# Kernel optimization log

Measured on AMD Instinct MI355X. Metric: run time of the kernel, lower is better.

## Reference

```python
import jax, jax.numpy as jnp
import numpy as np

N_EMBD = 1024
N_HEAD = 16
HEAD_DIM = N_EMBD // N_HEAD


def setup_inputs() -> dict:
    key = jax.random.key(0)
    ks = jax.random.split(key, 5)
    B, S = 2, 2048
    scale = 0.02
    return {
        "hidden_states": jax.random.normal(ks[0], (B, S, N_EMBD), dtype=jnp.float32),
        "w_attn": jax.random.normal(ks[1], (N_EMBD, 3 * N_EMBD), dtype=jnp.float32) * scale,
        "b_attn": jnp.zeros((3 * N_EMBD,), dtype=jnp.float32),
        "w_proj": jax.random.normal(ks[2], (N_EMBD, N_EMBD), dtype=jnp.float32) * scale,
        "b_proj": jnp.zeros((N_EMBD,), dtype=jnp.float32),
    }


def reference(hidden_states, w_attn, b_attn, w_proj, b_proj):
    B, S, _ = hidden_states.shape
    qkv = hidden_states @ w_attn + b_attn                     # [B,S,3E]
    q, k, v = jnp.split(qkv, 3, axis=-1)                      # each [B,S,E]

    def split_heads(t):  # [B,S,E] -> [B,H,S,D]
        return t.reshape(B, S, N_HEAD, HEAD_DIM).transpose(0, 2, 1, 3)

    q, k, v = split_heads(q), split_heads(k), split_heads(v)

    scores = jnp.einsum("bhqd,bhkd->bhqk", q, k) / np.sqrt(HEAD_DIM).astype(np.float32)
    causal = jnp.tril(jnp.ones((S, S), dtype=bool))
    scores = jnp.where(causal[None, None], scores, jnp.float32(-jnp.inf))
    attn = jax.nn.softmax(scores, axis=-1)                    # [B,H,S,S]
    out = jnp.einsum("bhqk,bhkd->bhqd", attn, v)              # [B,H,S,D]
    out = out.transpose(0, 2, 1, 3).reshape(B, S, N_EMBD)     # merge heads
    out = out @ w_proj + b_proj
    return out
```

## Files before the change

### kernel.cpp

```cpp
#include <hip/hip_runtime.h>
#include <hip/hip_bf16.h>


typedef __attribute__((ext_vector_type(4))) float  float4v;
typedef __attribute__((ext_vector_type(8))) short  short8v;
typedef __attribute__((ext_vector_type(4))) short  short4v;

#define ATT_SCALE 0.18033688011112042f

__device__ __forceinline__ short f2bf(float f) {
  union { float f; unsigned u; } v; v.f = f;
  unsigned r = v.u + 0x7fffu + ((v.u >> 16) & 1u);
  return (short)(r >> 16);
}
__device__ __forceinline__ float bf2f(short s) {
  union { unsigned u; float f; } v; v.u = ((unsigned)(unsigned short)s) << 16;
  return v.f;
}

__device__ __forceinline__ short4v pack_bf16x4(float a, float b, float c, float d) {
  unsigned x0 = __builtin_bit_cast(unsigned, a) + 0x8000u;
  unsigned x1 = __builtin_bit_cast(unsigned, b) + 0x8000u;
  unsigned x2 = __builtin_bit_cast(unsigned, c) + 0x8000u;
  unsigned x3 = __builtin_bit_cast(unsigned, d) + 0x8000u;
  union { unsigned u[2]; short4v s; } r;
  r.u[0] = __builtin_amdgcn_perm(x1, x0, 0x07060302);
  r.u[1] = __builtin_amdgcn_perm(x3, x2, 0x07060302);
  return r.s;
}

__device__ __forceinline__ short4v cvt_pk_bf16x4(float a, float b, float c, float d) {
  union { unsigned u[2]; short4v s; } r;
  asm("v_cvt_pk_bf16_f32 %0, %1, %2" : "=v"(r.u[0]) : "v"(a), "v"(b));
  asm("v_cvt_pk_bf16_f32 %0, %1, %2" : "=v"(r.u[1]) : "v"(c), "v"(d));
  return r.s;
}

__device__ __forceinline__ void gl_lds16(const void* g, void* l) {
  __builtin_amdgcn_global_load_lds(
      (const __attribute__((address_space(1))) unsigned*)g,
      (__attribute__((address_space(3))) unsigned*)l, 16, 0, 0);
}

__global__ __launch_bounds__(256) void prep_kernel(
    const float* __restrict__ hidden, const float* __restrict__ w_attn,
    const float* __restrict__ w_proj, short* __restrict__ hA,
    short* __restrict__ wqkvT, short* __restrict__ wprojT) {
  __shared__ float tile[32][33];
  const int bx = blockIdx.x, t = threadIdx.x;
  if (bx < 4096) {
    const size_t i = ((size_t)bx * 256 + t) * 4;
    float4v v = *(const float4v*)(hidden + i);
    short4v o;
    #pragma unroll
    for (int k = 0; k < 4; k++) o[k] = f2bf(v[k]);
    *(short4v*)(hA + i) = o;
    return;
  }
  const float* in; short* out; int R, C, cx, cy;
  if (bx < 4096 + 3072) {
    in = w_attn; out = wqkvT; R = 1024; C = 3072;
    cx = (bx - 4096) % 96; cy = (bx - 4096) / 96;
  } else {
    in = w_proj; out = wprojT; R = 1024; C = 1024;
    cx = (bx - 7168) % 32; cy = (bx - 7168) / 32;
  }
  const int tx = t & 31, ty = t >> 5;
  const int c0 = cx * 32, r0 = cy * 32;
  #pragma unroll
  for (int i = 0; i < 4; i++)
    tile[ty + i * 8][tx] = in[(size_t)(r0 + ty + i * 8) * C + c0 + tx];
  __syncthreads();
  #pragma unroll
  for (int i = 0; i < 4; i++) {
    const int cc = ty + i * 8;
    out[(size_t)(c0 + cc) * R + r0 + tx] = f2bf(tile[tx][cc]);
  }
}

__global__ __launch_bounds__(512, 2) void gemm_qkv256(
    const short* __restrict__ A, const short* __restrict__ Bt,
    const float* __restrict__ bias, short* __restrict__ qkv,
    short* __restrict__ vA)
{
  __shared__ short As[2][256][64];
  __shared__ short Bs[2][256][64];
  const int K = 1024;
  const int t = threadIdx.x;
  const int lane = t & 63, w = t >> 6;
  const int wm2 = w >> 2, wn4 = w & 3;
  const int l16 = lane & 15, quad = lane >> 4;
  const int e7 = l16 & 7;
  const int row0 = blockIdx.y * 256;
  const int col0 = blockIdx.x * 256;

  float4v acc[8][4] = {};

  const int srow = w * 8 + (lane >> 3);
  const int slog = (lane & 7) ^ (lane >> 3);
  const short* gA = A + (size_t)(row0 + srow) * K + slog * 8;
  const short* gB = Bt + (size_t)(col0 + srow) * K + slog * 8;
  const int sdst = (lane & 7) * 8;

  auto stageA = [&](int b, int qd, int kt) {
    gl_lds16(gA + (size_t)qd * 64 * K + kt * 64,
             &As[b][qd * 64 + w * 8 + (lane >> 3)][sdst]);
  };
  auto stageB = [&](int b, int qd, int kt) {
    gl_lds16(gB + (size_t)qd * 64 * K + kt * 64,
             &Bs[b][qd * 64 + w * 8 + (lane >> 3)][sdst]);
  };

  short8v af[4], bf0[4], bf1[4];
  auto ldA = [&](int b, int mh, int ks) {
    #pragma unroll
    for (int m = 0; m < 4; m++) {
      const int row = wm2 * 128 + mh * 64 + m * 16 + l16;
      af[m] = *(const short8v*)&As[b][row][((ks * 4 + quad) ^ e7) * 8];
    }
  };
  auto ldB = [&](short8v* bf, int b, int ks) {
    #pragma unroll
    for (int n = 0; n < 4; n++) {
      const int row = wn4 * 64 + n * 16 + l16;
      bf[n] = *(const short8v*)&Bs[b][row][((ks * 4 + quad) ^ e7) * 8];
    }
  };
  auto mm = [&](int mb, short8v* bf) {
    __builtin_amdgcn_s_setprio(1);
    #pragma unroll
    for (int m = 0; m < 4; m++)
      #pragma unroll
      for (int n = 0; n < 4; n++)
        acc[mb + m][n] =
            __builtin_amdgcn_mfma_f32_16x16x32_bf16(af[m], bf[n], acc[mb + m][n], 0, 0, 0);
    __builtin_amdgcn_s_setprio(0);
  };
  auto sync_mfma = [&]() {
    __builtin_amdgcn_sched_barrier(0);
    __builtin_amdgcn_s_barrier();
    asm volatile("s_waitcnt lgkmcnt(0)" ::: "memory");
    __builtin_amdgcn_sched_barrier(0);
  };
  auto endp = [&]() {
    __builtin_amdgcn_sched_barrier(0);
    __builtin_amdgcn_s_barrier();
    __builtin_amdgcn_sched_barrier(0);
  };

  #pragma unroll
  for (int qd = 0; qd < 4; qd++) stageA(0, qd, 0);
  #pragma unroll
  for (int qd = 0; qd < 4; qd++) stageB(0, qd, 0);
  #pragma unroll
  for (int qd = 0; qd < 4; qd++) stageB(1, qd, 1);
  asm volatile("s_waitcnt vmcnt(4)" ::: "memory");
  __builtin_amdgcn_s_barrier();
  __builtin_amdgcn_sched_barrier(0);

  const int NIT = K / 128;
  #pragma unroll 1
  for (int it = 0; it < NIT; it++) {
    const bool st = (it < NIT - 1);
    const int t1 = 2 * it + 1, t2 = 2 * it + 2, t3 = 2 * it + 3;

    ldA(0, 0, 0); ldB(bf0, 0, 0);
    stageA(1, 0, t1); stageA(1, 1, t1);
    sync_mfma(); mm(0, bf0); endp();
    ldA(0, 0, 1); ldB(bf1, 0, 1);
    stageA(1, 2, t1); stageA(1, 3, t1);
    sync_mfma(); mm(0, bf1); endp();
    ldA(0, 1, 0);
    if (st) { stageB(0, 0, t2); stageB(0, 1, t2); }
    sync_mfma(); mm(4, bf0); endp();
    ldA(0, 1, 1);
    if (st) { stageB(0, 2, t2); stageB(0, 3, t2); }
    if (st) asm volatile("s_waitcnt vmcnt(4)" ::: "memory");
    else    asm volatile("s_waitcnt vmcnt(0)" ::: "memory");
    sync_mfma(); mm(4, bf1); endp();

    ldA(1, 0, 0); ldB(bf0, 1, 0);
    if (st) { stageA(0, 0, t2); stageA(0, 1, t2); }
    sync_mfma(); mm(0, bf0); endp();
    ldA(1, 0, 1); ldB(bf1, 1, 1);
    if (st) { stageA(0, 2, t2); stageA(0, 3, t2); }
    sync_mfma(); mm(0, bf1); endp();
    ldA(1, 1, 0);
    if (st) { stageB(1, 0, t3); stageB(1, 1, t3); }
    sync_mfma(); mm(4, bf0); endp();
    ldA(1, 1, 1);
    if (st) { stageB(1, 2, t3); stageB(1, 3, t3); }
    if (st) asm volatile("s_waitcnt vmcnt(4)" ::: "memory");
    sync_mfma(); mm(4, bf1); endp();
  }

  if (col0 >= 2048) {
    const int b  = row0 >> 11;
    const int hh = ((col0 - 2048) >> 6) + wn4;
    #pragma unroll
    for (int ktl = 0; ktl < 2; ktl++) {
      const int kt = ((row0 & 2047) >> 6) + wm2 * 2 + ktl;
      short* vbase = vA + ((size_t)((b * 16 + hh) * 32 + kt) * 8) * 512;
      #pragma unroll
      for (int j = 0; j < 4; j++) {
        const float bv = bias[col0 + wn4 * 64 + j * 16 + l16];
        #pragma unroll
        for (int kwp = 0; kwp < 2; kwp++) {
          short8v s8;
          #pragma unroll
          for (int kw = 0; kw < 2; kw++) {
            const int mi = ktl * 4 + kwp * 2 + kw;
            short4v q4 = pack_bf16x4(acc[mi][j][0] + bv, acc[mi][j][1] + bv,
                                     acc[mi][j][2] + bv, acc[mi][j][3] + bv);
            #pragma unroll
            for (int r = 0; r < 4; r++) s8[kw * 4 + r] = q4[r];
          }
          *(short8v*)(vbase + ((size_t)(kwp * 4 + j) * 64 + lane) * 8) = s8;
        }
      }
    }
    return;
  }
  #pragma unroll
  for (int j = 0; j < 4; j++) {
    const int col = col0 + wn4 * 64 + j * 16 + l16;
    const float sc = (col < 1024) ? ATT_SCALE : 1.0f;
    const float bv = bias[col];
    #pragma unroll
    for (int mi = 0; mi < 8; mi++) {
      #pragma unroll
      for (int r = 0; r < 4; r++) {
        const int row = row0 + wm2 * 128 + mi * 16 + quad * 4 + r;
        qkv[(size_t)row * 3072 + col] = f2bf((acc[mi][j][r] + bv) * sc);
      }
    }
  }
}

__global__ __launch_bounds__(256, 2) void gemm_proj128(
    const short* __restrict__ A, const short* __restrict__ Bt,
    const float* __restrict__ bias, float* __restrict__ Cout)
{
  __shared__ short As[2][128][64];
  __shared__ short Bs[2][128][64];
  const int K = 1024;
  const int t = threadIdx.x;
  const int lane = t & 63, w = t >> 6;
  const int wm2 = w >> 1, wn2 = w & 1;
  const int l16 = lane & 15, quad = lane >> 4;
  const int e7 = l16 & 7;
  const int row0 = blockIdx.y * 128;
  const int col0 = blockIdx.x * 128;

  float4v acc[4][4] = {};

  const int srow = w * 8 + (lane >> 3);
  const int slog = (lane & 7) ^ (lane >> 3);
  const short* gA = A + (size_t)(row0 + srow) * K + slog * 8;
  const short* gB = Bt + (size_t)(col0 + srow) * K + slog * 8;
  const int sdst = (lane & 7) * 8;

  auto stageA = [&](int b, int qd, int kt) {
    gl_lds16(gA + (size_t)qd * 32 * K + kt * 64,
             &As[b][qd * 32 + w * 8 + (lane >> 3)][sdst]);
  };
  auto stageB = [&](int b, int qd, int kt) {
    gl_lds16(gB + (size_t)qd * 32 * K + kt * 64,
             &Bs[b][qd * 32 + w * 8 + (lane >> 3)][sdst]);
  };

  short8v af[2], bf0[4], bf1[4];
  auto ldA = [&](int b, int mh, int ks) {
    #pragma unroll
    for (int m = 0; m < 2; m++) {
      const int row = wm2 * 64 + mh * 32 + m * 16 + l16;
      af[m] = *(const short8v*)&As[b][row][((ks * 4 + quad) ^ e7) * 8];
    }
  };
  auto ldB = [&](short8v* bf, int b, int ks) {
    #pragma unroll
    for (int n = 0; n < 4; n++) {
      const int row = wn2 * 64 + n * 16 + l16;
      bf[n] = *(const short8v*)&Bs[b][row][((ks * 4 + quad) ^ e7) * 8];
    }
  };
  auto mm = [&](int mb, short8v* bf) {
    __builtin_amdgcn_s_setprio(1);
    #pragma unroll
    for (int m = 0; m < 2; m++)
      #pragma unroll
      for (int n = 0; n < 4; n++)
        acc[mb + m][n] =
            __builtin_amdgcn_mfma_f32_16x16x32_bf16(af[m], bf[n], acc[mb + m][n], 0, 0, 0);
    __builtin_amdgcn_s_setprio(0);
  };
  auto sync_mfma = [&]() {
    __builtin_amdgcn_sched_barrier(0);
    __builtin_amdgcn_s_barrier();
    asm volatile("s_waitcnt lgkmcnt(0)" ::: "memory");
    __builtin_amdgcn_sched_barrier(0);
  };
  auto endp = [&]() {
    __builtin_amdgcn_sched_barrier(0);
    __builtin_amdgcn_s_barrier();
    __builtin_amdgcn_sched_barrier(0);
  };

  #pragma unroll
  for (int qd = 0; qd < 4; qd++) stageA(0, qd, 0);
  #pragma unroll
  for (int qd = 0; qd < 4; qd++) stageB(0, qd, 0);
  #pragma unroll
  for (int qd = 0; qd < 4; qd++) stageB(1, qd, 1);
  asm volatile("s_waitcnt vmcnt(4)" ::: "memory");
  __builtin_amdgcn_s_barrier();
  __builtin_amdgcn_sched_barrier(0);

  const int NIT = K / 128;
  #pragma unroll 1
  for (int it = 0; it < NIT; it++) {
    const bool st = (it < NIT - 1);
    const int t1 = 2 * it + 1, t2 = 2 * it + 2, t3 = 2 * it + 3;

    ldA(0, 0, 0); ldB(bf0, 0, 0);
    stageA(1, 0, t1); stageA(1, 1, t1);
    sync_mfma(); mm(0, bf0); endp();
    ldA(0, 0, 1); ldB(bf1, 0, 1);
    stageA(1, 2, t1); stageA(1, 3, t1);
    sync_mfma(); mm(0, bf1); endp();
    ldA(0, 1, 0);
    if (st) { stageB(0, 0, t2); stageB(0, 1, t2); }
    sync_mfma(); mm(2, bf0); endp();
    ldA(0, 1, 1);
    if (st) { stageB(0, 2, t2); stageB(0, 3, t2); }
    if (st) asm volatile("s_waitcnt vmcnt(4)" ::: "memory");
    else    asm volatile("s_waitcnt vmcnt(0)" ::: "memory");
    sync_mfma(); mm(2, bf1); endp();

    ldA(1, 0, 0); ldB(bf0, 1, 0);
    if (st) { stageA(0, 0, t2); stageA(0, 1, t2); }
    sync_mfma(); mm(0, bf0); endp();
    ldA(1, 0, 1); ldB(bf1, 1, 1);
    if (st) { stageA(0, 2, t2); stageA(0, 3, t2); }
    sync_mfma(); mm(0, bf1); endp();
    ldA(1, 1, 0);
    if (st) { stageB(1, 0, t3); stageB(1, 1, t3); }
    sync_mfma(); mm(2, bf0); endp();
    ldA(1, 1, 1);
    if (st) { stageB(1, 2, t3); stageB(1, 3, t3); }
    if (st) asm volatile("s_waitcnt vmcnt(4)" ::: "memory");
    sync_mfma(); mm(2, bf1); endp();
  }

  #pragma unroll
  for (int j = 0; j < 4; j++) {
    const int col = col0 + wn2 * 64 + j * 16 + l16;
    const float bv = bias[col];
    #pragma unroll
    for (int mi = 0; mi < 4; mi++) {
      #pragma unroll
      for (int r = 0; r < 4; r++) {
        const int row = row0 + wm2 * 64 + mi * 16 + quad * 4 + r;
        Cout[(size_t)row * 1024 + col] = acc[mi][j][r] + bv;
      }
    }
  }
}

__global__ __launch_bounds__(64, 2) void attn_mfma(
    const short* __restrict__ qkv, const short* __restrict__ vA,
    short* __restrict__ P0, short* __restrict__ P1, float* __restrict__ lp)
{
  const int bh = blockIdx.x;
  const int b = bh >> 4, h = bh & 15;
  const int s = 79 - blockIdx.y;
  int qt = 0, sbase = 0;
  for (;;) { const int nc = (qt >> 3) + 1; if (s < sbase + nc) break; sbase += nc; qt++; }
  const int c = s - sbase;
  const int kt0  = c * 8;
  const int kend = min(qt + 1, kt0 + 8);

  const int lane = threadIdx.x & 63;
  const int l16 = lane & 15, quad = lane >> 4;

  const size_t base = (size_t)b * 2048 * 3072;
  const int qoff = h * 64, koff = 1024 + h * 64;

  int qg[4];
  short8v qf[4][2];
  #pragma unroll
  for (int hh = 0; hh < 4; hh++) {
    qg[hh] = qt * 64 + hh * 16 + l16;
    #pragma unroll
    for (int ks = 0; ks < 2; ks++)
      qf[hh][ks] = *(const short8v*)(qkv + base + (size_t)qg[hh] * 3072
                                     + qoff + ks * 32 + quad * 8);
  }

  float4v O[4][4] = {};
  float l[4] = {0.0f, 0.0f, 0.0f, 0.0f};

  const short* kg = qkv + base + (size_t)l16 * 3072 + koff + quad * 8;
  const short* vg = vA + (size_t)(bh * 32) * 4096 + lane * 8;

  for (int kt = kt0; kt < kend; kt++) {
    short8v kf[8];
    #pragma unroll
    for (int id = 0; id < 8; id++)
      kf[id] = *(const short8v*)(kg + ((size_t)kt * 64 + (id & 3) * 16) * 3072
                                    + (id >> 2) * 32);
    short8v vv[8];
    #pragma unroll
    for (int id = 0; id < 8; id++)
      vv[id] = *(const short8v*)(vg + (size_t)kt * 4096 + id * 512);

    short4v pk[4][4];
    #pragma unroll
    for (int jm = 0; jm < 4; jm++) {
      float4v sv[4] = {};
      __builtin_amdgcn_s_setprio(1);
      #pragma unroll
      for (int hh = 0; hh < 4; hh++)
        sv[hh] = __builtin_amdgcn_mfma_f32_16x16x32_bf16(kf[jm], qf[hh][0],
                                                         sv[hh], 0, 0, 0);
      #pragma unroll
      for (int hh = 0; hh < 4; hh++)
        sv[hh] = __builtin_amdgcn_mfma_f32_16x16x32_bf16(kf[4 + jm], qf[hh][1],
                                                         sv[hh], 0, 0, 0);
      __builtin_amdgcn_s_setprio(0);

      if (kt == qt) {
        const int kv = kt * 64 + jm * 16 + quad * 4;
        #pragma unroll
        for (int hh = 0; hh < 4; hh++)
          #pragma unroll
          for (int r = 0; r < 4; r++)
            if (kv + r > qg[hh]) sv[hh][r] = -INFINITY;
      }

      #pragma unroll
      for (int hh = 0; hh < 4; hh++) {
        float p0 = __builtin_amdgcn_exp2f(sv[hh][0]);
        float p1 = __builtin_amdgcn_exp2f(sv[hh][1]);
        float p2 = __builtin_amdgcn_exp2f(sv[hh][2]);
        float p3 = __builtin_amdgcn_exp2f(sv[hh][3]);
        l[hh] += (p0 + p1) + (p2 + p3);
        pk[hh][jm] = cvt_pk_bf16x4(p0, p1, p2, p3);
      }
    }

    __builtin_amdgcn_s_setprio(1);
    #pragma unroll
    for (int id = 0; id < 8; id++) {
      const int kwp = id >> 2, dm = id & 3;
      const short8v v8 = vv[id];
      const short4v v0 = {v8[0], v8[1], v8[2], v8[3]};
      const short4v v1 = {v8[4], v8[5], v8[6], v8[7]};
      #pragma unroll
      for (int hh = 0; hh < 4; hh++) {
        O[hh][dm] = __builtin_amdgcn_mfma_f32_16x16x16bf16_1k(v0, pk[hh][kwp * 2],
                                                              O[hh][dm], 0, 0, 0);
        O[hh][dm] = __builtin_amdgcn_mfma_f32_16x16x16bf16_1k(v1, pk[hh][kwp * 2 + 1],
                                                              O[hh][dm], 0, 0, 0);
      }
    }
    __builtin_amdgcn_s_setprio(0);
  }

  #pragma unroll
  for (int hh = 0; hh < 4; hh++) {
    l[hh] += __shfl_xor(l[hh], 16);
    l[hh] += __shfl_xor(l[hh], 32);
  }
  const int i = bh * 80 + s;
  short* pp = (i < 2048) ? (P0 + (size_t)i * 4096) : (P1 + (size_t)(i - 2048) * 4096);
  #pragma unroll
  for (int hh = 0; hh < 4; hh++) {
    const int row = hh * 16 + l16;
    if (quad == 0) lp[(size_t)i * 64 + row] = l[hh];
    short* pr = pp + row * 64;
    #pragma unroll
    for (int dm = 0; dm < 4; dm++)
      *(short4v*)(pr + dm * 16 + quad * 4) =
          pack_bf16x4(O[hh][dm][0], O[hh][dm][1], O[hh][dm][2], O[hh][dm][3]);
  }
}

__global__ __launch_bounds__(256) void merge_attn(
    const short* __restrict__ P0, const short* __restrict__ P1,
    const float* __restrict__ lp, short* __restrict__ aout)
{
  const int idx = blockIdx.x * 256 + threadIdx.x;
  const int q = idx >> 7;
  const int rest = idx & 127;
  const int h  = rest >> 3;
  const int dg = (rest & 7) * 8;
  const int b  = q >> 11;
  const int qr = q & 2047;
  const int qt = qr >> 6;
  const int row = qr & 63;
  const int a = qt >> 3, bq = qt & 7;
  const int off = qt + 4 * a * (a - 1) + a * bq;
  const int nc  = a + 1;
  const int bh  = b * 16 + h;

  float acc[8] = {};
  float suml = 0.0f;
  for (int c = 0; c < nc; c++) {
    const int i = bh * 80 + off + c;
    const short* pp = (i < 2048) ? (P0 + (size_t)i * 4096) : (P1 + (size_t)(i - 2048) * 4096);
    const short8v o = *(const short8v*)(pp + row * 64 + dg);
    #pragma unroll
    for (int k = 0; k < 8; k++) acc[k] += bf2f(o[k]);
    suml += lp[(size_t)i * 64 + row];
  }
  const float inv = 1.0f / suml;
  short8v ov;
  #pragma unroll
  for (int k = 0; k < 8; k++) ov[k] = f2bf(acc[k] * inv);
  *(short8v*)(aout + (size_t)q * 1024 + h * 64 + dg) = ov;
}

extern "C" void kernel_launch(void* const* d_in, const int* in_sizes, int n_in,
                              void* d_out, int out_size, void* d_ws, size_t ws_size,
                              hipStream_t stream) {
  const float* hidden = (const float*)d_in[0];
  const float* w_attn = (const float*)d_in[1];
  const float* b_attn = (const float*)d_in[2];
  const float* w_proj = (const float*)d_in[3];
  const float* b_proj = (const float*)d_in[4];
  float* outp = (float*)d_out;

  char* ws = (char*)d_ws;
  short* hA     = (short*)(ws);
  float* lp     = (float*)(ws + 8ull  * 1024 * 1024);
  short* wqkvT  = (short*)(ws + 8ull  * 1024 * 1024);
  short* wprojT = (short*)(ws + 14ull * 1024 * 1024);
  short* qkvb   = (short*)(ws + 16ull * 1024 * 1024);
  short* vAbuf  = (short*)(ws + 40ull * 1024 * 1024);
  short* aout   = (short*)(ws + 40ull * 1024 * 1024);
  short* P0     = (short*)d_out;

  prep_kernel<<<8192, 256, 0, stream>>>(hidden, w_attn, w_proj, hA, wqkvT, wprojT);
  gemm_qkv256<<<dim3(12, 16), 512, 0, stream>>>(hA, wqkvT, b_attn, qkvb, vAbuf);
  attn_mfma<<<dim3(32, 80), 64, 0, stream>>>(qkvb, vAbuf, P0, hA, lp);
  merge_attn<<<2048, 256, 0, stream>>>(P0, hA, lp, aout);
  gemm_proj128<<<dim3(8, 32), 256, 0, stream>>>(aout, wprojT, b_proj, outp);
}
```

Measured before the change: 188.1 us.

## Stage QKV GEMM epilogue through LDS for coalesced stores and remap block order

Merges the A/B shared buffers into one flat LDS array so the epilogue can reuse it. Converted Q/K outputs are written into LDS with an XOR swizzle and then stored to global memory as 16-byte row-contiguous vectors, instead of scattered 2-byte strided stores. Block IDs are also remapped so consecutive workgroups walk down row tiles of the same column strip, which should improve L2 reuse of B. The cost is two extra barriers and an LDS round trip in the epilogue.

```diff
diff --git a/kernel.cpp b/kernel.cpp
--- a/kernel.cpp
+++ b/kernel.cpp
@@ -83,16 +83,18 @@
     const float* __restrict__ bias, short* __restrict__ qkv,
     short* __restrict__ vA)
 {
-  __shared__ short As[2][256][64];
-  __shared__ short Bs[2][256][64];
+  __shared__ short LDSH[65536];
   const int K = 1024;
   const int t = threadIdx.x;
   const int lane = t & 63, w = t >> 6;
   const int wm2 = w >> 2, wn4 = w & 3;
   const int l16 = lane & 15, quad = lane >> 4;
   const int e7 = l16 & 7;
-  const int row0 = blockIdx.y * 256;
-  const int col0 = blockIdx.x * 256;
+
+  const int bid  = blockIdx.y * 12 + blockIdx.x;
+  const int wgid = (bid & 7) * 24 + (bid >> 3);
+  const int row0 = (wgid & 15) * 256;
+  const int col0 = (wgid >> 4) * 256;
 
   float4v acc[8][4] = {};
 
@@ -104,11 +106,11 @@
 
   auto stageA = [&](int b, int qd, int kt) {
     gl_lds16(gA + (size_t)qd * 64 * K + kt * 64,
-             &As[b][qd * 64 + w * 8 + (lane >> 3)][sdst]);
+             &LDSH[b * 16384 + (qd * 64 + w * 8 + (lane >> 3)) * 64 + sdst]);
   };
   auto stageB = [&](int b, int qd, int kt) {
     gl_lds16(gB + (size_t)qd * 64 * K + kt * 64,
-             &Bs[b][qd * 64 + w * 8 + (lane >> 3)][sdst]);
+             &LDSH[32768 + b * 16384 + (qd * 64 + w * 8 + (lane >> 3)) * 64 + sdst]);
   };
 
   short8v af[4], bf0[4], bf1[4];
@@ -116,14 +118,14 @@
     #pragma unroll
     for (int m = 0; m < 4; m++) {
       const int row = wm2 * 128 + mh * 64 + m * 16 + l16;
-      af[m] = *(const short8v*)&As[b][row][((ks * 4 + quad) ^ e7) * 8];
+      af[m] = *(const short8v*)&LDSH[b * 16384 + row * 64 + ((ks * 4 + quad) ^ e7) * 8];
     }
   };
   auto ldB = [&](short8v* bf, int b, int ks) {
     #pragma unroll
     for (int n = 0; n < 4; n++) {
       const int row = wn4 * 64 + n * 16 + l16;
-      bf[n] = *(const short8v*)&Bs[b][row][((ks * 4 + quad) ^ e7) * 8];
+      bf[n] = *(const short8v*)&LDSH[32768 + b * 16384 + row * 64 + ((ks * 4 + quad) ^ e7) * 8];
     }
   };
   auto mm = [&](int mb, short8v* bf) {
@@ -221,19 +223,31 @@
     }
     return;
   }
+
+  __syncthreads();
   #pragma unroll
   for (int j = 0; j < 4; j++) {
-    const int col = col0 + wn4 * 64 + j * 16 + l16;
-    const float sc = (col < 1024) ? ATT_SCALE : 1.0f;
-    const float bv = bias[col];
+    const int col = wn4 * 64 + j * 16 + l16;
+    const float sc = (col0 + col < 1024) ? ATT_SCALE : 1.0f;
+    const float bv = bias[col0 + col];
     #pragma unroll
     for (int mi = 0; mi < 8; mi++) {
-      #pragma unroll
-      for (int r = 0; r < 4; r++) {
-        const int row = row0 + wm2 * 128 + mi * 16 + quad * 4 + r;
-        qkv[(size_t)row * 3072 + col] = f2bf((acc[mi][j][r] + bv) * sc);
-      }
-    }
+      const int rowb = wm2 * 128 + mi * 16 + quad * 4;
+      const int key = ((rowb >> 2) & 3) << 4;
+      #pragma unroll
+      for (int r = 0; r < 4; r++)
+        LDSH[(rowb + r) * 256 + (col ^ key)] = f2bf((acc[mi][j][r] + bv) * sc);
+    }
+  }
+  __syncthreads();
+  #pragma unroll
+  for (int p = 0; p < 16; p++) {
+    const int idx = p * 512 + t;
+    const int r   = idx >> 5;
+    const int c8  = (idx & 31) << 3;
+    const int cp  = c8 ^ (((r >> 2) & 3) << 4);
+    const short8v v = *(const short8v*)&LDSH[r * 256 + cp];
+    *(short8v*)(qkv + (size_t)(row0 + r) * 3072 + col0 + c8) = v;
   }
 }
 
```

New measurement: 184.2 us (median of 2 runs). -2.1%, faster.

## Shrink QKV GEMM tile to 128x128, remap blocks, stage Q/K output through LDS

Applied to the files above, without the earlier changes.

The QKV projection GEMM moves from 256x256 tiles with 512 threads to 128x128 tiles with 256 threads, giving 768 workgroups instead of 192 and filling the 256 CUs more evenly. Workgroup IDs are remapped so consecutive blocks spread across column tiles in groups of 8. The Q/K epilogue now writes results into XOR-swizzled LDS and then issues coalesced 16-byte row stores, replacing scattered 2-byte global writes. Smaller tiles lower arithmetic intensity and add more global/L2 traffic for A and B.

```diff
diff --git a/kernel.cpp b/kernel.cpp
--- a/kernel.cpp
+++ b/kernel.cpp
@@ -78,23 +78,25 @@
   }
 }
 
-__global__ __launch_bounds__(512, 2) void gemm_qkv256(
+__global__ __launch_bounds__(256, 2) void gemm_qkv128(
     const short* __restrict__ A, const short* __restrict__ Bt,
     const float* __restrict__ bias, short* __restrict__ qkv,
     short* __restrict__ vA)
 {
-  __shared__ short As[2][256][64];
-  __shared__ short Bs[2][256][64];
+  __shared__ short LDSH[32768];
   const int K = 1024;
   const int t = threadIdx.x;
   const int lane = t & 63, w = t >> 6;
-  const int wm2 = w >> 2, wn4 = w & 3;
+  const int wm2 = w >> 1, wn2 = w & 1;
   const int l16 = lane & 15, quad = lane >> 4;
   const int e7 = l16 & 7;
-  const int row0 = blockIdx.y * 256;
-  const int col0 = blockIdx.x * 256;
-
-  float4v acc[8][4] = {};
+
+  const int bid  = blockIdx.y * 24 + blockIdx.x;
+  const int wgid = (bid & 7) * 96 + (bid >> 3);
+  const int row0 = (wgid & 31) * 128;
+  const int col0 = (wgid >> 5) * 128;
+
+  float4v acc[4][4] = {};
 
   const int srow = w * 8 + (lane >> 3);
   const int slog = (lane & 7) ^ (lane >> 3);
@@ -103,33 +105,33 @@
   const int sdst = (lane & 7) * 8;
 
   auto stageA = [&](int b, int qd, int kt) {
-    gl_lds16(gA + (size_t)qd * 64 * K + kt * 64,
-             &As[b][qd * 64 + w * 8 + (lane >> 3)][sdst]);
+    gl_lds16(gA + (size_t)qd * 32 * K + kt * 64,
+             &LDSH[b * 8192 + (qd * 32 + w * 8 + (lane >> 3)) * 64 + sdst]);
   };
   auto stageB = [&](int b, int qd, int kt) {
-    gl_lds16(gB + (size_t)qd * 64 * K + kt * 64,
-             &Bs[b][qd * 64 + w * 8 + (lane >> 3)][sdst]);
-  };
-
-  short8v af[4], bf0[4], bf1[4];
+    gl_lds16(gB + (size_t)qd * 32 * K + kt * 64,
+             &LDSH[16384 + b * 8192 + (qd * 32 + w * 8 + (lane >> 3)) * 64 + sdst]);
+  };
+
+  short8v af[2], bf0[4], bf1[4];
   auto ldA = [&](int b, int mh, int ks) {
     #pragma unroll
-    for (int m = 0; m < 4; m++) {
-      const int row = wm2 * 128 + mh * 64 + m * 16 + l16;
-      af[m] = *(const short8v*)&As[b][row][((ks * 4 + quad) ^ e7) * 8];
+    for (int m = 0; m < 2; m++) {
+      const int row = wm2 * 64 + mh * 32 + m * 16 + l16;
+      af[m] = *(const short8v*)&LDSH[b * 8192 + row * 64 + ((ks * 4 + quad) ^ e7) * 8];
     }
   };
   auto ldB = [&](short8v* bf, int b, int ks) {
     #pragma unroll
     for (int n = 0; n < 4; n++) {
-      const int row = wn4 * 64 + n * 16 + l16;
-      bf[n] = *(const short8v*)&Bs[b][row][((ks * 4 + quad) ^ e7) * 8];
+      const int row = wn2 * 64 + n * 16 + l16;
+      bf[n] = *(const short8v*)&LDSH[16384 + b * 8192 + row * 64 + ((ks * 4 + quad) ^ e7) * 8];
     }
   };
   auto mm = [&](int mb, short8v* bf) {
     __builtin_amdgcn_s_setprio(1);
     #pragma unroll
-    for (int m = 0; m < 4; m++)
+    for (int m = 0; m < 2; m++)
       #pragma unroll
       for (int n = 0; n < 4; n++)
         acc[mb + m][n] =
@@ -172,12 +174,12 @@
     sync_mfma(); mm(0, bf1); endp();
     ldA(0, 1, 0);
     if (st) { stageB(0, 0, t2); stageB(0, 1, t2); }
-    sync_mfma(); mm(4, bf0); endp();
+    sync_mfma(); mm(2, bf0); endp();
     ldA(0, 1, 1);
     if (st) { stageB(0, 2, t2); stageB(0, 3, t2); }
     if (st) asm volatile("s_waitcnt vmcnt(4)" ::: "memory");
     else    asm volatile("s_waitcnt vmcnt(0)" ::: "memory");
-    sync_mfma(); mm(4, bf1); endp();
+    sync_mfma(); mm(2, bf1); endp();
 
     ldA(1, 0, 0); ldB(bf0, 1, 0);
     if (st) { stageA(0, 0, t2); stageA(0, 1, t2); }
@@ -187,53 +189,64 @@
     sync_mfma(); mm(0, bf1); endp();
     ldA(1, 1, 0);
     if (st) { stageB(1, 0, t3); stageB(1, 1, t3); }
-    sync_mfma(); mm(4, bf0); endp();
+    sync_mfma(); mm(2, bf0); endp();
     ldA(1, 1, 1);
     if (st) { stageB(1, 2, t3); stageB(1, 3, t3); }
     if (st) asm volatile("s_waitcnt vmcnt(4)" ::: "memory");
-    sync_mfma(); mm(4, bf1); endp();
+    sync_mfma(); mm(2, bf1); endp();
   }
 
   if (col0 >= 2048) {
     const int b  = row0 >> 11;
-    const int hh = ((col0 - 2048) >> 6) + wn4;
-    #pragma unroll
-    for (int ktl = 0; ktl < 2; ktl++) {
-      const int kt = ((row0 & 2047) >> 6) + wm2 * 2 + ktl;
-      short* vbase = vA + ((size_t)((b * 16 + hh) * 32 + kt) * 8) * 512;
-      #pragma unroll
-      for (int j = 0; j < 4; j++) {
-        const float bv = bias[col0 + wn4 * 64 + j * 16 + l16];
+    const int hh = ((col0 - 2048) >> 6) + wn2;
+    const int kt = ((row0 & 2047) >> 6) + wm2;
+    short* vbase = vA + ((size_t)((b * 16 + hh) * 32 + kt) * 8) * 512;
+    #pragma unroll
+    for (int j = 0; j < 4; j++) {
+      const float bv = bias[col0 + wn2 * 64 + j * 16 + l16];
+      #pragma unroll
+      for (int kwp = 0; kwp < 2; kwp++) {
+        short8v s8;
         #pragma unroll
-        for (int kwp = 0; kwp < 2; kwp++) {
-          short8v s8;
+        for (int kw = 0; kw < 2; kw++) {
+          short4v q4 = pack_bf16x4(acc[kwp * 2 + kw][j][0] + bv,
+                                   acc[kwp * 2 + kw][j][1] + bv,
+                                   acc[kwp * 2 + kw][j][2] + bv,
+                                   acc[kwp * 2 + kw][j][3] + bv);
           #pragma unroll
-          for (int kw = 0; kw < 2; kw++) {
-            const int mi = ktl * 4 + kwp * 2 + kw;
-            short4v q4 = pack_bf16x4(acc[mi][j][0] + bv, acc[mi][j][1] + bv,
-                                     acc[mi][j][2] + bv, acc[mi][j][3] + bv);
-            #pragma unroll
-            for (int r = 0; r < 4; r++) s8[kw * 4 + r] = q4[r];
-          }
-          *(short8v*)(vbase + ((size_t)(kwp * 4 + j) * 64 + lane) * 8) = s8;
+          for (int r = 0; r < 4; r++) s8[kw * 4 + r] = q4[r];
         }
+        *(short8v*)(vbase + ((size_t)(kwp * 4 + j) * 64 + lane) * 8) = s8;
       }
     }
     return;
   }
+
+  __syncthreads();
   #pragma unroll
   for (int j = 0; j < 4; j++) {
-    const int col = col0 + wn4 * 64 + j * 16 + l16;
-    const float sc = (col < 1024) ? ATT_SCALE : 1.0f;
-    const float bv = bias[col];
-    #pragma unroll
-    for (int mi = 0; mi < 8; mi++) {
+    const int col = wn2 * 64 + j * 16 + l16;
+    const float sc = (col0 + col < 1024) ? ATT_SCALE : 1.0f;
+    const float bv = bias[col0 + col];
+    #pragma unroll
+    for (int mi = 0; mi < 4; mi++) {
+      const int rowb = wm2 * 64 + mi * 16 + quad * 4;
       #pragma unroll
       for (int r = 0; r < 4; r++) {
-        const int row = row0 + wm2 * 128 + mi * 16 + quad * 4 + r;
-        qkv[(size_t)row * 3072 + col] = f2bf((acc[mi][j][r] + bv) * sc);
+        const int key = (quad ^ r) << 4;
+        LDSH[(rowb + r) * 128 + (col ^ key)] = f2bf((acc[mi][j][r] + bv) * sc);
       }
     }
+  }
+  __syncthreads();
+  #pragma unroll
+  for (int p = 0; p < 8; p++) {
+    const int idx = p * 256 + t;
+    const int r   = idx >> 4;
+    const int c8  = (idx & 15) << 3;
+    const int cp  = c8 ^ (((((r >> 2) & 3) ^ (r & 3))) << 4);
+    const short8v v = *(const short8v*)&LDSH[r * 128 + cp];
+    *(short8v*)(qkv + (size_t)(row0 + r) * 3072 + col0 + c8) = v;
   }
 }
 
@@ -542,7 +555,7 @@
   short* P0     = (short*)d_out;
 
   prep_kernel<<<8192, 256, 0, stream>>>(hidden, w_attn, w_proj, hA, wqkvT, wprojT);
-  gemm_qkv256<<<dim3(12, 16), 512, 0, stream>>>(hA, wqkvT, b_attn, qkvb, vAbuf);
+  gemm_qkv128<<<dim3(24, 32), 256, 0, stream>>>(hA, wqkvT, b_attn, qkvb, vAbuf);
   attn_mfma<<<dim3(32, 80), 64, 0, stream>>>(qkvb, vAbuf, P0, hA, lp);
   merge_attn<<<2048, 256, 0, stream>>>(P0, hA, lp, aout);
   gemm_proj128<<<dim3(8, 32), 256, 0, stream>>>(aout, wprojT, b_proj, outp);
```

Measured after the change: 186.3 us. No clear change (-1.0%).
